# Optimization experiments

Hardware: AMD Instinct MI355X
Metric: run time of the kernel (lower is better)

## Reference

```python
import jax, jax.numpy as jnp
import numpy as np

B, T, C, H = 2, 2048, 1024, 16
D = C // H  # head_dim = 64


def setup_inputs() -> dict:
    key = jax.random.key(0)
    k1, k2, k3 = jax.random.split(key, 3)
    scale = 0.02
    return {
        "x": jax.random.normal(k1, (B, T, C), dtype=jnp.float32),
        "w_qkv": jax.random.normal(k2, (C, 3 * C), dtype=jnp.float32) * scale,
        "b_qkv": jnp.zeros((3 * C,), dtype=jnp.float32),
        "w_out": jax.random.normal(k3, (C, C), dtype=jnp.float32) * scale,
        "b_out": jnp.zeros((C,), dtype=jnp.float32),
    }


def reference(x, w_qkv, b_qkv, w_out, b_out):
    b, t, c = x.shape
    qkv = x @ w_qkv + b_qkv                       # [b, t, 3c]
    q, k, v = jnp.split(qkv, 3, axis=-1)
    # [b, t, c] -> [b, h, t, d]
    q = q.reshape(b, t, H, D).transpose(0, 2, 1, 3)
    k = k.reshape(b, t, H, D).transpose(0, 2, 1, 3)
    v = v.reshape(b, t, H, D).transpose(0, 2, 1, 3)
    scores = jnp.einsum("bhqd,bhkd->bhqk", q, k) / jnp.sqrt(jnp.asarray(D, dtype=q.dtype))
    causal = jnp.tril(jnp.ones((t, t), dtype=bool))
    scores = jnp.where(causal, scores, jnp.finfo(scores.dtype).min)
    attn = jax.nn.softmax(scores, axis=-1)        # [b, h, q, k]
    out = jnp.einsum("bhqk,bhkd->bhqd", attn, v)  # [b, h, t, d]
    out = out.transpose(0, 2, 1, 3).reshape(b, t, c)
    return out @ w_out + b_out
```

## Files before the change

### kernel.cpp

```cpp
#include <hip/hip_runtime.h>

#define B_ 2
#define T_ 2048
#define C_ 1024
#define H_ 16
#define D_ 64
#define MLS (32 * 16 * 64)

using bf16x8 = __attribute__((ext_vector_type(8))) short;
using f32x4  = __attribute__((ext_vector_type(4))) float;

static __device__ __forceinline__ short f2bf(float f) {
  unsigned u = __builtin_bit_cast(unsigned, f);
  unsigned r = u + 0x7fffu + ((u >> 16) & 1u);
  return (short)(r >> 16);
}

#define GLD16(gp, lp) __builtin_amdgcn_global_load_lds( \
    (const __attribute__((address_space(1))) void*)(gp), \
    (__attribute__((address_space(3))) void*)(lp), 16, 0, 0)

__global__ __launch_bounds__(256) void cast_f32_bf16(const float* __restrict__ in,
                                                     short* __restrict__ out) {
  int i = blockIdx.x * blockDim.x + threadIdx.x;
  float4 v = ((const float4*)in)[i];
  short4 o;
  o.x = f2bf(v.x); o.y = f2bf(v.y); o.z = f2bf(v.z); o.w = f2bf(v.w);
  ((short4*)out)[i] = o;
}

__global__ __launch_bounds__(256) void transpose_cast(const float* __restrict__ in,
                                                      short* __restrict__ out,
                                                      int R, int N) {
  __shared__ float tile[32][33];
  int bx = blockIdx.x * 32, by = blockIdx.y * 32;
  int tx = threadIdx.x, ty = threadIdx.y;
  #pragma unroll
  for (int j = 0; j < 32; j += 8)
    tile[ty + j][tx] = in[(size_t)(by + ty + j) * N + bx + tx];
  __syncthreads();
  #pragma unroll
  for (int j = 0; j < 32; j += 8)
    out[(size_t)(bx + ty + j) * R + by + tx] = f2bf(tile[tx][ty + j]);
}

__global__ __launch_bounds__(256) void gemm_qkv(const short* __restrict__ A,
                                                const short* __restrict__ Bt,
                                                const float* __restrict__ bias,
                                                short* __restrict__ Qo,
                                                short* __restrict__ Ko,
                                                short* __restrict__ Vo) {
  __shared__ short sA[128 * 64];
  __shared__ short sB[128 * 64];
  const int tid = threadIdx.x;
  const int w = tid >> 6, lane = tid & 63;
  const int wm = w >> 1, wn = w & 1;
  const int g = lane >> 4, r16 = lane & 15;
  const int m0 = blockIdx.x * 128, n0 = blockIdx.y * 128;
  const int krow = lane >> 3, kslot = lane & 7;

  f32x4 acc[4][4] = {};

  for (int k0 = 0; k0 < 1024; k0 += 64) {
    __syncthreads();
    #pragma unroll
    for (int p = 0; p < 4; ++p) {
      int rbase = w * 32 + p * 8;
      int row = rbase + krow;
      GLD16(&A[(size_t)(m0 + row) * 1024 + k0 + ((kslot ^ (row & 7)) * 8)], &sA[rbase * 64]);
      GLD16(&Bt[(size_t)(n0 + row) * 1024 + k0 + ((kslot ^ (row & 7)) * 8)], &sB[rbase * 64]);
    }
    __syncthreads();
    bf16x8 af[4][2], bf[4][2];
    #pragma unroll
    for (int mi = 0; mi < 4; ++mi) {
      int row = wm * 64 + mi * 16 + r16;
      #pragma unroll
      for (int c = 0; c < 2; ++c)
        af[mi][c] = *(const bf16x8*)&sA[row * 64 + (((c * 4 + g) ^ (row & 7)) * 8)];
    }
    #pragma unroll
    for (int ni = 0; ni < 4; ++ni) {
      int row = wn * 64 + ni * 16 + r16;
      #pragma unroll
      for (int c = 0; c < 2; ++c)
        bf[ni][c] = *(const bf16x8*)&sB[row * 64 + (((c * 4 + g) ^ (row & 7)) * 8)];
    }
    __builtin_amdgcn_s_setprio(1);
    #pragma unroll
    for (int mi = 0; mi < 4; ++mi)
      #pragma unroll
      for (int ni = 0; ni < 4; ++ni) {
        acc[mi][ni] = __builtin_amdgcn_mfma_f32_16x16x32_bf16(af[mi][0], bf[ni][0], acc[mi][ni], 0, 0, 0);
        acc[mi][ni] = __builtin_amdgcn_mfma_f32_16x16x32_bf16(af[mi][1], bf[ni][1], acc[mi][ni], 0, 0, 0);
      }
    __builtin_amdgcn_s_setprio(0);
  }

  #pragma unroll
  for (int mi = 0; mi < 4; ++mi) {
    #pragma unroll
    for (int ni = 0; ni < 4; ++ni) {
      int n = n0 + wn * 64 + ni * 16 + r16;
      float bv = bias[n];
      int which = n >> 10;
      int c = n & 1023;
      int hh = c >> 6, d = c & 63;
      short* dst = (which == 0) ? Qo : ((which == 1) ? Ko : Vo);
      float sc = (which == 0) ? 0.18033688f : 1.0f;
      #pragma unroll
      for (int rr = 0; rr < 4; ++rr) {
        int m = m0 + wm * 64 + mi * 16 + g * 4 + rr;
        int b = m >> 11, t = m & 2047;
        dst[(size_t)((b * H_ + hh) * T_ + t) * D_ + d] = f2bf((acc[mi][ni][rr] + bv) * sc);
      }
    }
  }
}

__global__ __launch_bounds__(256) void gemm_out(const short* __restrict__ A,
                                                const short* __restrict__ Bt,
                                                const float* __restrict__ bias,
                                                float* __restrict__ Out) {
  __shared__ short sA[128 * 64];
  __shared__ short sB[64 * 64];
  const int tid = threadIdx.x;
  const int w = tid >> 6, lane = tid & 63;
  const int wm = w >> 1, wn = w & 1;
  const int g = lane >> 4, r16 = lane & 15;
  const int m0 = blockIdx.x * 128, n0 = blockIdx.y * 64;
  const int krow = lane >> 3, kslot = lane & 7;

  f32x4 acc[4][2] = {};

  for (int k0 = 0; k0 < 1024; k0 += 64) {
    __syncthreads();
    #pragma unroll
    for (int p = 0; p < 4; ++p) {
      int rbase = w * 32 + p * 8;
      int row = rbase + krow;
      GLD16(&A[(size_t)(m0 + row) * 1024 + k0 + ((kslot ^ (row & 7)) * 8)], &sA[rbase * 64]);
    }
    #pragma unroll
    for (int p = 0; p < 2; ++p) {
      int rbase = w * 16 + p * 8;
      int row = rbase + krow;
      GLD16(&Bt[(size_t)(n0 + row) * 1024 + k0 + ((kslot ^ (row & 7)) * 8)], &sB[rbase * 64]);
    }
    __syncthreads();
    bf16x8 af[4][2], bf[2][2];
    #pragma unroll
    for (int mi = 0; mi < 4; ++mi) {
      int row = wm * 64 + mi * 16 + r16;
      #pragma unroll
      for (int c = 0; c < 2; ++c)
        af[mi][c] = *(const bf16x8*)&sA[row * 64 + (((c * 4 + g) ^ (row & 7)) * 8)];
    }
    #pragma unroll
    for (int ni = 0; ni < 2; ++ni) {
      int row = wn * 32 + ni * 16 + r16;
      #pragma unroll
      for (int c = 0; c < 2; ++c)
        bf[ni][c] = *(const bf16x8*)&sB[row * 64 + (((c * 4 + g) ^ (row & 7)) * 8)];
    }
    __builtin_amdgcn_s_setprio(1);
    #pragma unroll
    for (int mi = 0; mi < 4; ++mi)
      #pragma unroll
      for (int ni = 0; ni < 2; ++ni) {
        acc[mi][ni] = __builtin_amdgcn_mfma_f32_16x16x32_bf16(af[mi][0], bf[ni][0], acc[mi][ni], 0, 0, 0);
        acc[mi][ni] = __builtin_amdgcn_mfma_f32_16x16x32_bf16(af[mi][1], bf[ni][1], acc[mi][ni], 0, 0, 0);
      }
    __builtin_amdgcn_s_setprio(0);
  }

  #pragma unroll
  for (int mi = 0; mi < 4; ++mi) {
    #pragma unroll
    for (int ni = 0; ni < 2; ++ni) {
      int n = n0 + wn * 32 + ni * 16 + r16;
      float bv = bias[n];
      #pragma unroll
      for (int rr = 0; rr < 4; ++rr) {
        int m = m0 + wm * 64 + mi * 16 + g * 4 + rr;
        Out[(size_t)m * 1024 + n] = acc[mi][ni][rr] + bv;
      }
    }
  }
}

__global__ __launch_bounds__(256, 4) void attn_fwd(const short* __restrict__ Q,
                                                   const short* __restrict__ K,
                                                   const short* __restrict__ V,
                                                   short* __restrict__ O,
                                                   short* __restrict__ part,
                                                   float* __restrict__ ml) {
  __shared__ short sK[2][64 * 64];
  __shared__ short vT[2][64 * 64];

  const int tid = threadIdx.x;
  const int w = tid >> 6, lane = tid & 63;
  const int g = lane >> 4, r16 = lane & 15;
  const int bh = blockIdx.x;
  const int b = bh >> 4, hh = bh & 15;
  const int yy = blockIdx.y;
  const int k3 = yy / 3, r3 = yy - 3 * k3;
  const int split = (r3 != 2);
  const int qi = split ? (31 - k3) : (15 - k3);
  const int half = split ? r3 : 0;
  const int q0 = qi * 64;
  const int kt0 = (split && half) ? ((qi + 1) >> 1) : 0;
  const int kt1 = (split && !half) ? ((qi + 1) >> 1) : (qi + 1);

  const short* Qh = Q + (size_t)bh * T_ * D_;
  const short* Kh = K + (size_t)bh * T_ * D_;
  const short* Vh = V + (size_t)bh * T_ * D_;

  const int krow_in_wave = lane >> 3;
  const int kslot = lane & 7;
  const int kp = tid & 31;
  const int vd0 = (tid >> 5) * 8;
  const int vchunk = (kp >> 4) * 4 + ((kp & 7) >> 1);
  const int velem  = ((kp >> 3) & 1) * 4 + 2 * (kp & 1);

  const int qrow_a = q0 + w * 16 + r16;
  bf16x8 qf[2];
  qf[0] = *(const bf16x8*)&Qh[(size_t)qrow_a * 64 + g * 8];
  qf[1] = *(const bf16x8*)&Qh[(size_t)qrow_a * 64 + 32 + g * 8];

  f32x4 o[4] = {};
  float m_ = -1e30f, l_ = 0.f;

  #pragma unroll
  for (int p = 0; p < 2; ++p) {
    int row = w * 16 + p * 8 + krow_in_wave;
    GLD16(&Kh[(size_t)(kt0 * 64 + row) * 64 + ((kslot ^ (row & 7)) * 8)],
          &sK[0][(w * 16 + p * 8) * 64]);
  }
  {
    int4 v0 = *(const int4*)&Vh[(size_t)(kt0 * 64 + 2 * kp) * 64 + vd0];
    int4 v1 = *(const int4*)&Vh[(size_t)(kt0 * 64 + 2 * kp + 1) * 64 + vd0];
    const short* a0 = (const short*)&v0;
    const short* a1 = (const short*)&v1;
    #pragma unroll
    for (int j = 0; j < 8; ++j) {
      int d = vd0 + j;
      int val = ((int)(unsigned short)a0[j]) | (((int)(unsigned short)a1[j]) << 16);
      *(int*)&vT[0][d * 64 + ((vchunk ^ j) * 8) + velem] = val;
    }
  }
  __syncthreads();

  for (int kt = kt0; kt < kt1; ++kt) {
    const int cur = (kt - kt0) & 1, nxt = cur ^ 1;
    const int k0 = kt * 64;
    const bool pf = (kt + 1 < kt1);

    int4 vn0, vn1;
    if (pf) {
      const int k1 = k0 + 64;
      #pragma unroll
      for (int p = 0; p < 2; ++p) {
        int row = w * 16 + p * 8 + krow_in_wave;
        GLD16(&Kh[(size_t)(k1 + row) * 64 + ((kslot ^ (row & 7)) * 8)],
              &sK[nxt][(w * 16 + p * 8) * 64]);
      }
      vn0 = *(const int4*)&Vh[(size_t)(k1 + 2 * kp) * 64 + vd0];
      vn1 = *(const int4*)&Vh[(size_t)(k1 + 2 * kp + 1) * 64 + vd0];
    }

    f32x4 s[4] = {};
    __builtin_amdgcn_s_setprio(1);
    #pragma unroll
    for (int nt = 0; nt < 4; ++nt) {
      const int row = nt * 16 + r16;
      const int sw8 = r16 & 7;
      bf16x8 kf0 = *(const bf16x8*)&sK[cur][row * 64 + ((g ^ sw8) * 8)];
      bf16x8 kf1 = *(const bf16x8*)&sK[cur][row * 64 + (((4 + g) ^ sw8) * 8)];
      s[nt] = __builtin_amdgcn_mfma_f32_16x16x32_bf16(kf0, qf[0], s[nt], 0, 0, 0);
      s[nt] = __builtin_amdgcn_mfma_f32_16x16x32_bf16(kf1, qf[1], s[nt], 0, 0, 0);
    }
    __builtin_amdgcn_s_setprio(0);

    if (kt == qi) {
      const int qrow = w * 16 + r16;
      #pragma unroll
      for (int nt = 0; nt < 4; ++nt)
        #pragma unroll
        for (int rr = 0; rr < 4; ++rr)
          if (nt * 16 + 4 * g + rr > qrow) s[nt][rr] = -1e30f;
    }
    float pmax = s[0][0];
    #pragma unroll
    for (int nt = 0; nt < 4; ++nt)
      #pragma unroll
      for (int rr = 0; rr < 4; ++rr)
        pmax = fmaxf(pmax, s[nt][rr]);
    if (!__all(pmax - m_ <= 8.0f)) {
      float rmax = fmaxf(pmax, __shfl_xor(pmax, 16));
      rmax = fmaxf(rmax, __shfl_xor(rmax, 32));
      float mn = fmaxf(m_, rmax);
      float al = __builtin_amdgcn_exp2f(m_ - mn);
      m_ = mn;
      l_ *= al;
      float av[4];
      #pragma unroll
      for (int rr = 0; rr < 4; ++rr) av[rr] = __shfl(al, 4 * g + rr, 16);
      #pragma unroll
      for (int nt = 0; nt < 4; ++nt)
        #pragma unroll
        for (int rr = 0; rr < 4; ++rr) o[nt][rr] *= av[rr];
    }
    float rs = 0.f;
    #pragma unroll
    for (int nt = 0; nt < 4; ++nt)
      #pragma unroll
      for (int rr = 0; rr < 4; ++rr) {
        float p = __builtin_amdgcn_exp2f(s[nt][rr] - m_);
        s[nt][rr] = p;
        rs += p;
      }
    l_ += rs;
    int pk[8];
    #pragma unroll
    for (int nt = 0; nt < 4; ++nt)
      #pragma unroll
      for (int h = 0; h < 2; ++h)
        asm("v_cvt_pk_bf16_f32 %0, %1, %2"
            : "=v"(pk[nt * 2 + h])
            : "v"(s[nt][2 * h]), "v"(s[nt][2 * h + 1]));

    bf16x8 pa[2];
    {
      int4 t0; t0.x = pk[0]; t0.y = pk[1]; t0.z = pk[2]; t0.w = pk[3];
      int4 t1; t1.x = pk[4]; t1.y = pk[5]; t1.z = pk[6]; t1.w = pk[7];
      pa[0] = __builtin_bit_cast(bf16x8, t0);
      pa[1] = __builtin_bit_cast(bf16x8, t1);
    }
    __builtin_amdgcn_s_setprio(1);
    #pragma unroll
    for (int nt = 0; nt < 4; ++nt) {
      const int d = nt * 16 + r16;
      bf16x8 vb0 = *(const bf16x8*)&vT[cur][d * 64 + ((g ^ (d & 7)) * 8)];
      bf16x8 vb1 = *(const bf16x8*)&vT[cur][d * 64 + (((4 + g) ^ (d & 7)) * 8)];
      o[nt] = __builtin_amdgcn_mfma_f32_16x16x32_bf16(pa[0], vb0, o[nt], 0, 0, 0);
      o[nt] = __builtin_amdgcn_mfma_f32_16x16x32_bf16(pa[1], vb1, o[nt], 0, 0, 0);
    }
    __builtin_amdgcn_s_setprio(0);

    if (pf) {
      const short* a0 = (const short*)&vn0;
      const short* a1 = (const short*)&vn1;
      #pragma unroll
      for (int j = 0; j < 8; ++j) {
        int d = vd0 + j;
        int val = ((int)(unsigned short)a0[j]) | (((int)(unsigned short)a1[j]) << 16);
        *(int*)&vT[nxt][d * 64 + ((vchunk ^ j) * 8) + velem] = val;
      }
    }
    __syncthreads();
  }

  float lt = l_ + __shfl_xor(l_, 16);
  lt += __shfl_xor(lt, 32);
  float lv[4];
  #pragma unroll
  for (int rr = 0; rr < 4; ++rr) lv[rr] = __shfl(lt, 4 * g + rr, 16);

  if (!split || half == 0) {
    #pragma unroll
    for (int nt = 0; nt < 4; ++nt) {
      int d = nt * 16 + r16;
      #pragma unroll
      for (int rr = 0; rr < 4; ++rr) {
        int t = q0 + w * 16 + 4 * g + rr;
        O[(size_t)(b * T_ + t) * C_ + hh * 64 + d] = f2bf(o[nt][rr] / lv[rr]);
      }
    }
  } else {
    const int p = qi - 16;
    #pragma unroll
    for (int nt = 0; nt < 4; ++nt) {
      int d = nt * 16 + r16;
      #pragma unroll
      for (int rr = 0; rr < 4; ++rr) {
        int row = w * 16 + 4 * g + rr;
        part[((size_t)((bh * 16 + p) * 64 + row)) * 64 + d] = f2bf(o[nt][rr] / lv[rr]);
      }
    }
  }
  if (split && lane < 16) {
    const int p = qi - 16;
    int mi = (bh * 16 + p) * 64 + w * 16 + lane;
    ml[half * MLS + mi] = m_;
    ml[(2 + half) * MLS + mi] = lt;
  }
}

__global__ __launch_bounds__(256) void attn_combine(const short* __restrict__ part,
                                                    const float* __restrict__ ml,
                                                    short* __restrict__ O) {
  const int bh = blockIdx.x, p = blockIdx.y;
  const int qi = 16 + p;
  const int b = bh >> 4, hh = bh & 15;
  const int tid = threadIdx.x;
  const int row = tid >> 2;
  const int d0 = (tid & 3) * 16;
  const int mi = (bh * 16 + p) * 64 + row;
  float m1 = ml[mi],           m2 = ml[MLS + mi];
  float l1 = ml[2 * MLS + mi], l2 = ml[3 * MLS + mi];
  float ms = fmaxf(m1, m2);
  float w1 = l1 * __builtin_amdgcn_exp2f(m1 - ms);
  float w2 = l2 * __builtin_amdgcn_exp2f(m2 - ms);
  float inv = 1.0f / (w1 + w2);
  w1 *= inv; w2 *= inv;
  short* op = O + ((size_t)(b * T_ + qi * 64 + row) * C_) + hh * 64 + d0;
  const short* pp = part + ((size_t)((bh * 16 + p) * 64 + row)) * 64 + d0;
  #pragma unroll
  for (int v = 0; v < 2; ++v) {
    int4 a = *(const int4*)(op + v * 8);
    int4 c = *(const int4*)(pp + v * 8);
    const short* as = (const short*)&a;
    const short* cs = (const short*)&c;
    short r[8];
    #pragma unroll
    for (int j = 0; j < 8; ++j) {
      float o1 = __builtin_bit_cast(float, ((unsigned)(unsigned short)as[j]) << 16);
      float o2 = __builtin_bit_cast(float, ((unsigned)(unsigned short)cs[j]) << 16);
      r[j] = f2bf(w1 * o1 + w2 * o2);
    }
    *(int4*)(op + v * 8) = *(int4*)r;
  }
}

extern "C" void kernel_launch(void* const* d_in, const int* in_sizes, int n_in,
                              void* d_out, int out_size, void* d_ws, size_t ws_size,
                              hipStream_t stream) {
  const float* x     = (const float*)d_in[0];
  const float* w_qkv = (const float*)d_in[1];
  const float* b_qkv = (const float*)d_in[2];
  const float* w_out = (const float*)d_in[3];
  const float* b_out = (const float*)d_in[4];
  float* out = (float*)d_out;

  char* ws = (char*)d_ws;
  if (ws_size < (size_t)(40u << 20)) return;

  short* xb     = (short*)(ws);
  short* wqkvT  = (short*)(ws + ((size_t)8u << 20));
  short* woutT  = (short*)(ws + ((size_t)14u << 20));
  short* Qb     = (short*)(ws + ((size_t)16u << 20));
  short* Kb     = (short*)(ws + ((size_t)24u << 20));
  short* Vb     = (short*)(ws + ((size_t)32u << 20));
  short* attn_o = xb;
  short* part   = wqkvT;
  float* ml     = (float*)(ws + ((size_t)12u << 20));

  cast_f32_bf16<<<4096, 256, 0, stream>>>(x, xb);
  transpose_cast<<<dim3(96, 32), dim3(32, 8), 0, stream>>>(w_qkv, wqkvT, 1024, 3072);
  transpose_cast<<<dim3(32, 32), dim3(32, 8), 0, stream>>>(w_out, woutT, 1024, 1024);
  gemm_qkv<<<dim3(32, 24), 256, 0, stream>>>(xb, wqkvT, b_qkv, Qb, Kb, Vb);
  attn_fwd<<<dim3(32, 48), 256, 0, stream>>>(Qb, Kb, Vb, attn_o, part, ml);
  attn_combine<<<dim3(32, 16), 256, 0, stream>>>(part, ml, attn_o);
  gemm_out<<<dim3(32, 16), 256, 0, stream>>>(attn_o, woutT, b_out, out);
}
```

Baseline: 118.9 us.

## Write V transposed from QKV GEMM and load it directly into LDS

The QKV GEMM epilogue for the V columns now stages the tile in shared memory and writes V in a per-head [D, T] transposed layout with coalesced stores. The attention kernel then loads V tiles with async global-to-LDS copies in the same swizzled pattern as K, instead of register loads followed by per-element transposing LDS writes each iteration. This removes per-iteration VALU and LDS shuffle work from the attention loop. In exchange the GEMM epilogue gains extra barriers and a larger shared buffer, which may reduce its occupancy.

New measurement: 112.0 us. -5.7%, faster.

```diff
diff --git a/kernel.cpp b/kernel.cpp
--- a/kernel.cpp
+++ b/kernel.cpp
@@ -49,9 +49,10 @@
                                                 const float* __restrict__ bias,
                                                 short* __restrict__ Qo,
                                                 short* __restrict__ Ko,
-                                                short* __restrict__ Vo) {
-  __shared__ short sA[128 * 64];
-  __shared__ short sB[128 * 64];
+                                                short* __restrict__ Vt) {
+  __shared__ short smem[128 * 132];
+  short* sA = smem;
+  short* sB = smem + 128 * 64;
   const int tid = threadIdx.x;
   const int w = tid >> 6, lane = tid & 63;
   const int wm = w >> 1, wn = w & 1;
@@ -97,23 +98,52 @@
     __builtin_amdgcn_s_setprio(0);
   }
 
-  #pragma unroll
-  for (int mi = 0; mi < 4; ++mi) {
-    #pragma unroll
-    for (int ni = 0; ni < 4; ++ni) {
-      int n = n0 + wn * 64 + ni * 16 + r16;
-      float bv = bias[n];
-      int which = n >> 10;
-      int c = n & 1023;
-      int hh = c >> 6, d = c & 63;
-      short* dst = (which == 0) ? Qo : ((which == 1) ? Ko : Vo);
-      float sc = (which == 0) ? 0.18033688f : 1.0f;
-      #pragma unroll
-      for (int rr = 0; rr < 4; ++rr) {
-        int m = m0 + wm * 64 + mi * 16 + g * 4 + rr;
-        int b = m >> 11, t = m & 2047;
-        dst[(size_t)((b * H_ + hh) * T_ + t) * D_ + d] = f2bf((acc[mi][ni][rr] + bv) * sc);
-      }
+  if (n0 < 2048) {
+    const int which = n0 >> 10;
+    short* dst = (which == 0) ? Qo : Ko;
+    const float sc = (which == 0) ? 0.18033688f : 1.0f;
+    #pragma unroll
+    for (int mi = 0; mi < 4; ++mi) {
+      #pragma unroll
+      for (int ni = 0; ni < 4; ++ni) {
+        int n = n0 + wn * 64 + ni * 16 + r16;
+        float bv = bias[n];
+        int c = n & 1023;
+        int hh = c >> 6, d = c & 63;
+        #pragma unroll
+        for (int rr = 0; rr < 4; ++rr) {
+          int m = m0 + wm * 64 + mi * 16 + g * 4 + rr;
+          int b = m >> 11, t = m & 2047;
+          dst[(size_t)((b * H_ + hh) * T_ + t) * D_ + d] = f2bf((acc[mi][ni][rr] + bv) * sc);
+        }
+      }
+    }
+  } else {
+    __syncthreads();
+    #pragma unroll
+    for (int mi = 0; mi < 4; ++mi) {
+      #pragma unroll
+      for (int ni = 0; ni < 4; ++ni) {
+        int nn = wn * 64 + ni * 16 + r16;
+        float bv = bias[n0 + nn];
+        #pragma unroll
+        for (int rr = 0; rr < 4; ++rr) {
+          int tm = wm * 64 + mi * 16 + g * 4 + rr;
+          smem[tm * 132 + nn] = f2bf(acc[mi][ni][rr] + bv);
+        }
+      }
+    }
+    __syncthreads();
+    const int tinv = (lane & ~0x1C) | ((lane & 0x18) >> 1) | ((lane & 4) << 2);
+    const int b2 = m0 >> 11, t0l = m0 & 2047;
+    const int head0 = b2 * H_ + ((n0 - 2048) >> 6);
+    #pragma unroll 8
+    for (int i = 0; i < 64; ++i) {
+      int half = i >> 5, nnl = i & 31;
+      int nn = w * 32 + nnl;
+      int d = nn & 63, hh2 = nn >> 6;
+      short val = smem[(half * 64 + tinv) * 132 + nn];
+      Vt[((size_t)(head0 + hh2) * D_ + d) * T_ + t0l + half * 64 + lane] = val;
     }
   }
 }
@@ -191,7 +221,7 @@
 
 __global__ __launch_bounds__(256, 4) void attn_fwd(const short* __restrict__ Q,
                                                    const short* __restrict__ K,
-                                                   const short* __restrict__ V,
+                                                   const short* __restrict__ Vt,
                                                    short* __restrict__ O,
                                                    short* __restrict__ part,
                                                    float* __restrict__ ml) {
@@ -214,14 +244,10 @@
 
   const short* Qh = Q + (size_t)bh * T_ * D_;
   const short* Kh = K + (size_t)bh * T_ * D_;
-  const short* Vh = V + (size_t)bh * T_ * D_;
-
-  const int krow_in_wave = lane >> 3;
+  const short* Vh = Vt + (size_t)bh * D_ * T_;
+
+  const int krw = lane >> 3;
   const int kslot = lane & 7;
-  const int kp = tid & 31;
-  const int vd0 = (tid >> 5) * 8;
-  const int vchunk = (kp >> 4) * 4 + ((kp & 7) >> 1);
-  const int velem  = ((kp >> 3) & 1) * 4 + 2 * (kp & 1);
 
   const int qrow_a = q0 + w * 16 + r16;
   bf16x8 qf[2];
@@ -231,22 +257,16 @@
   f32x4 o[4] = {};
   float m_ = -1e30f, l_ = 0.f;
 
-  #pragma unroll
-  for (int p = 0; p < 2; ++p) {
-    int row = w * 16 + p * 8 + krow_in_wave;
-    GLD16(&Kh[(size_t)(kt0 * 64 + row) * 64 + ((kslot ^ (row & 7)) * 8)],
-          &sK[0][(w * 16 + p * 8) * 64]);
-  }
+
   {
-    int4 v0 = *(const int4*)&Vh[(size_t)(kt0 * 64 + 2 * kp) * 64 + vd0];
-    int4 v1 = *(const int4*)&Vh[(size_t)(kt0 * 64 + 2 * kp + 1) * 64 + vd0];
-    const short* a0 = (const short*)&v0;
-    const short* a1 = (const short*)&v1;
-    #pragma unroll
-    for (int j = 0; j < 8; ++j) {
-      int d = vd0 + j;
-      int val = ((int)(unsigned short)a0[j]) | (((int)(unsigned short)a1[j]) << 16);
-      *(int*)&vT[0][d * 64 + ((vchunk ^ j) * 8) + velem] = val;
+    const int k0 = kt0 * 64;
+    #pragma unroll
+    for (int p = 0; p < 2; ++p) {
+      int row = w * 16 + p * 8 + krw;
+      GLD16(&Kh[(size_t)(k0 + row) * 64 + ((kslot ^ (row & 7)) * 8)],
+            &sK[0][(w * 16 + p * 8) * 64]);
+      GLD16(&Vh[(size_t)row * T_ + k0 + ((kslot ^ (row & 7)) * 8)],
+            &vT[0][(w * 16 + p * 8) * 64]);
     }
   }
   __syncthreads();
@@ -256,17 +276,16 @@
     const int k0 = kt * 64;
     const bool pf = (kt + 1 < kt1);
 
-    int4 vn0, vn1;
     if (pf) {
       const int k1 = k0 + 64;
       #pragma unroll
       for (int p = 0; p < 2; ++p) {
-        int row = w * 16 + p * 8 + krow_in_wave;
+        int row = w * 16 + p * 8 + krw;
         GLD16(&Kh[(size_t)(k1 + row) * 64 + ((kslot ^ (row & 7)) * 8)],
               &sK[nxt][(w * 16 + p * 8) * 64]);
-      }
-      vn0 = *(const int4*)&Vh[(size_t)(k1 + 2 * kp) * 64 + vd0];
-      vn1 = *(const int4*)&Vh[(size_t)(k1 + 2 * kp + 1) * 64 + vd0];
+        GLD16(&Vh[(size_t)row * T_ + k1 + ((kslot ^ (row & 7)) * 8)],
+              &vT[nxt][(w * 16 + p * 8) * 64]);
+      }
     }
 
     f32x4 s[4] = {};
@@ -348,16 +367,6 @@
     }
     __builtin_amdgcn_s_setprio(0);
 
-    if (pf) {
-      const short* a0 = (const short*)&vn0;
-      const short* a1 = (const short*)&vn1;
-      #pragma unroll
-      for (int j = 0; j < 8; ++j) {
-        int d = vd0 + j;
-        int val = ((int)(unsigned short)a0[j]) | (((int)(unsigned short)a1[j]) << 16);
-        *(int*)&vT[nxt][d * 64 + ((vchunk ^ j) * 8) + velem] = val;
-      }
-    }
     __syncthreads();
   }
 
@@ -451,7 +460,7 @@
   short* woutT  = (short*)(ws + ((size_t)14u << 20));
   short* Qb     = (short*)(ws + ((size_t)16u << 20));
   short* Kb     = (short*)(ws + ((size_t)24u << 20));
-  short* Vb     = (short*)(ws + ((size_t)32u << 20));
+  short* Vtb    = (short*)(ws + ((size_t)32u << 20));
   short* attn_o = xb;
   short* part   = wqkvT;
   float* ml     = (float*)(ws + ((size_t)12u << 20));
@@ -459,8 +468,8 @@
   cast_f32_bf16<<<4096, 256, 0, stream>>>(x, xb);
   transpose_cast<<<dim3(96, 32), dim3(32, 8), 0, stream>>>(w_qkv, wqkvT, 1024, 3072);
   transpose_cast<<<dim3(32, 32), dim3(32, 8), 0, stream>>>(w_out, woutT, 1024, 1024);
-  gemm_qkv<<<dim3(32, 24), 256, 0, stream>>>(xb, wqkvT, b_qkv, Qb, Kb, Vb);
-  attn_fwd<<<dim3(32, 48), 256, 0, stream>>>(Qb, Kb, Vb, attn_o, part, ml);
+  gemm_qkv<<<dim3(32, 24), 256, 0, stream>>>(xb, wqkvT, b_qkv, Qb, Kb, Vtb);
+  attn_fwd<<<dim3(32, 48), 256, 0, stream>>>(Qb, Kb, Vtb, attn_o, part, ml);
   attn_combine<<<dim3(32, 16), 256, 0, stream>>>(part, ml, attn_o);
   gemm_out<<<dim3(32, 16), 256, 0, stream>>>(attn_o, woutT, b_out, out);
 }
```
